# Kernel tuning notes

Hardware: AMD Instinct MI355X
Metric: run time of the kernel (lower is better)

The kernel has to match this reference:

```python
import jax, jax.numpy as jnp
import numpy as np

ZERO = 1e-8
L = 2            # num_gnn_layers
D = 256          # dim_node_features
B = 32           # graphs per batch
NPG = 256        # nodes per graph
N = B * NPG      # total nodes
E = 131072       # edges per edge-type
MAX_TOKENS = 256 # MAX_TOKENS_OF_A_POST
UPD = 0.5        # args.updated_weights_for_A


def _make_edges(k):
    k1, k2, k3 = jax.random.split(k, 3)
    g = jax.random.randint(k1, (E,), 0, B) * NPG          # keep edges within a graph
    src = g + jax.random.randint(k2, (E,), 0, NPG)
    dst = g + jax.random.randint(k3, (E,), 0, NPG)
    return jnp.stack([src, dst]).astype(jnp.int64)


def setup_inputs() -> dict:
    key = jax.random.key(0)
    ks = jax.random.split(key, 12)
    x = jax.random.normal(ks[0], (N, D), dtype=jnp.float32)
    ei_e = _make_edges(ks[1]); ew_e = jax.random.uniform(ks[2], (E,), dtype=jnp.float32)
    ei_p = _make_edges(ks[3]); ew_p = jax.random.uniform(ks[4], (E,), dtype=jnp.float32)
    ei_o = _make_edges(ks[5]); ew_o = jax.random.uniform(ks[6], (E,), dtype=jnp.float32)
    entity_mask = jax.random.randint(ks[7], (B, NPG), 0, 2).astype(bool)
    pattern_mask = jax.random.randint(ks[8], (B, NPG), 0, 2).astype(bool)
    s = 1.0 / np.sqrt(D)
    W_gcn = (jax.random.normal(ks[9], (L, 3, D, D), dtype=jnp.float32) * s)
    b_gcn = jnp.zeros((L, 3, D), dtype=jnp.float32)
    T_dyn = (jax.random.normal(ks[10], (L, D, D), dtype=jnp.float32) * s)
    return {
        'x': x,
        'edge_index_entity': ei_e, 'edge_weight_entity': ew_e,
        'edge_index_pattern': ei_p, 'edge_weight_pattern': ew_p,
        'edge_index_others': ei_o, 'edge_weight_others': ew_o,
        'entity_mask': entity_mask, 'pattern_mask': pattern_mask,
        'W_gcn': W_gcn, 'b_gcn': b_gcn, 'T_dyn': T_dyn,
    }


def _normalized_correlation_matrix(H):
    # cosine-similarity correlation matrix, symmetrically degree-normalized
    nrm = jnp.sqrt(jnp.sum(H * H, axis=1))
    A = (H @ H.T) / (nrm[:, None] * nrm[None, :] + ZERO)
    dinv = 1.0 / jnp.sqrt(jnp.abs(jnp.sum(A, axis=1)) + ZERO)
    return dinv[:, None] * A * dinv[None, :]


def _gcn(H, W, b, ei, ew):
    # GCNConv(add_self_loops=False, normalize=False): scatter-sum of weighted source messages
    msg = (H @ W)[ei[0]] * ew[:, None]                     # [E, D]
    return jax.ops.segment_sum(msg, ei[1], num_segments=N) + b


def _forward(x, we0, wp0, wo0, W_gcn, b_gcn, T_dyn,
             ei_e, ei_p, ei_o, entity_mask, pattern_mask):
    H = x
    A = _normalized_correlation_matrix(H)                  # [N, N]
    for i in range(L):
        if i == 0:
            we, wp, wo = we0, wp0, wo0
        else:
            # diag(one_hot(src) @ A @ one_hot(dst).T) == A[src, dst]
            we = A[ei_e[0], ei_e[1]]
            wp = A[ei_p[0], ei_p[1]]
            wo = A[ei_o[0], ei_o[1]]
        He = _gcn(H, W_gcn[i, 0], b_gcn[i, 0], ei_e, we)
        Hp = _gcn(H, W_gcn[i, 1], b_gcn[i, 1], ei_p, wp)
        Ho = _gcn(H, W_gcn[i, 2], b_gcn[i, 2], ei_o, wo)
        H = jax.nn.relu(He + Hp + Ho)
        A_hat = jax.nn.sigmoid((H @ T_dyn[i]) @ H.T)
        A = (1.0 - UPD) * A + UPD * A_hat
    # per-graph diagonal blocks of A  -> [B, NPG, NPG]
    A4 = A.reshape(B, NPG, B, NPG)
    idx = jnp.arange(B)
    blocks = A4[idx, :, idx, :]
    A_sum = jnp.sum(blocks, axis=-1)                       # [B, NPG]
    ent_cols = jnp.einsum('bij,bj->bi', blocks, entity_mask.astype(A.dtype))
    pat_cols = jnp.einsum('bij,bj->bi', blocks, pattern_mask.astype(A.dtype))
    map_pattern = A_sum - ent_cols
    map_entity = A_sum - pat_cols

    def finish(m):
        mn = jnp.min(m, axis=1, keepdims=True)
        mx = jnp.max(m, axis=1, keepdims=True)
        m = (m - mn) / (mx - mn + ZERO)
        m = m / (jnp.sum(m, axis=1, keepdims=True) + ZERO)
        return m[:, :MAX_TOKENS]                           # padding() with NPG==MAX_TOKENS

    return finish(map_entity), finish(map_pattern)


def reference(x, edge_index_entity, edge_weight_entity,
              edge_index_pattern, edge_weight_pattern,
              edge_index_others, edge_weight_others,
              entity_mask, pattern_mask, W_gcn, b_gcn, T_dyn):
    return _forward(x, edge_weight_entity, edge_weight_pattern, edge_weight_others,
                    W_gcn, b_gcn, T_dyn,
                    edge_index_entity, edge_index_pattern, edge_index_others,
                    entity_mask, pattern_mask)
```

## Files before the change

### kernel.cpp

```cpp
#include <hip/hip_runtime.h>

#define NND   8192
#define DDIM  256
#define NGRP  32
#define ZEROF 1e-8f
#define LSTR  40
#define TSTR  72
#define OFF_AH 0
#define OFF_AL 2560
#define OFF_BH 5120
#define OFF_BL 10240
#define OFF_TT 5120
#define LDS_U16 15360

typedef unsigned short u16;
typedef __attribute__((ext_vector_type(8))) short short8v;
typedef __attribute__((ext_vector_type(4))) float float4v;

__device__ inline u16 f2bf(float x) {
  unsigned u = __float_as_uint(x);
  u += 0x7fffu + ((u >> 16) & 1u);
  return (u16)(u >> 16);
}
__device__ inline float bf2f(u16 h) { return __uint_as_float((unsigned)h << 16); }
__device__ inline void split2(float x, u16& h, u16& l) {
  h = f2bf(x);
  l = f2bf(x - bf2f(h));
}

__device__ inline float wave_sum(float v) {
#pragma unroll
  for (int off = 32; off > 0; off >>= 1) v += __shfl_down(v, off, 64);
  return v;
}

#define LOAD_REGS(tt, kk)                                                                   \
  {                                                                                         \
    int m_ = tid >> 2, kq_ = (tid & 3) * 8;                                                 \
    size_t aoff_;                                                                           \
    if (MODE == 1)                                                                          \
      aoff_ = (size_t)((tt) * 256 + bym * 64 + m_) * 8192 + (size_t)(g * 256 + (kk) + kq_); \
    else if (MODE == 2 || MODE == 3)                                                        \
      aoff_ = (size_t)(g * 256 + bym * 64 + m_) * 256 + (kk) + kq_;                         \
    else                                                                                    \
      aoff_ = (size_t)(bym * 64 + m_) * 256 + (kk) + kq_;                                   \
    rAh = *(const short8v*)&Ah_g[aoff_];                                                    \
    rAl = *(const short8v*)&Al_g[aoff_];                                                    \
    if (MODE == 1) {                                                                        \
      int n_ = tid >> 2, kq2_ = (tid & 3) * 8;                                              \
      const float* pb_ = Bfp + (((size_t)g * 3 + (tt)) << 16) +                             \
                         (size_t)(col0 + n_) * 256 + (kk) + kq2_;                           \
      rBf[0] = *(const float4*)pb_;                                                         \
      rBf[1] = *(const float4*)(pb_ + 4);                                                   \
    } else if (HALF) {                                                                      \
      int n_ = tid & 63, kq2_ = (tid >> 6) * 8;                                             \
      size_t boff_ = (size_t)(((MODE == 2 || MODE == 3) ? g * 256 : 0) + col0 + n_) * 256   \
                     + (kk) + kq2_;                                                         \
      rBh0 = *(const short8v*)&Bh_g[boff_];                                                 \
      rBl0 = *(const short8v*)&Bl_g[boff_];                                                 \
    } else {                                                                                \
      int n_ = tid & 127, kq2_ = (tid >> 7) * 16;                                           \
      size_t boff_ = (size_t)(col0 + n_) * 256 + (kk) + kq2_;                               \
      rBh0 = *(const short8v*)&Bh_g[boff_]; rBh1 = *(const short8v*)&Bh_g[boff_ + 8];       \
      rBl0 = *(const short8v*)&Bl_g[boff_]; rBl1 = *(const short8v*)&Bl_g[boff_ + 8];       \
    }                                                                                       \
  }

template<int MODE, bool HALF>
__device__ __forceinline__ void mfma_body(
    u16* lds,
    const u16* __restrict__ Ah_g, const u16* __restrict__ Al_g,
    const u16* __restrict__ Bh_g, const u16* __restrict__ Bl_g,
    const float* __restrict__ Bfp,
    float* __restrict__ Cf, u16* __restrict__ Ch, u16* __restrict__ Cl,
    const float* __restrict__ nrm, const float* __restrict__ dinv,
    const float* __restrict__ bias,
    int bxm, int bym, int g) {
  u16* Ahs = lds + OFF_AH;
  u16* Als = lds + OFF_AL;
  u16* Bhs = lds + OFF_BH;
  u16* Bls = lds + OFF_BL;
  u16* Tt  = lds + OFF_TT;
  const int NJ = HALF ? 2 : 4;
  const int tid = threadIdx.x;
  const int col0 = bxm * (HALF ? 64 : 128);
  const int w = tid >> 6, lane = tid & 63;
  const int lm = lane & 15, lq = lane >> 4;
  const int wr = (w >> 1) * 32, wc = (w & 1) * (HALF ? 32 : 64);

  float4v acc[2][4];
#pragma unroll
  for (int i = 0; i < 2; ++i)
#pragma unroll
    for (int j = 0; j < NJ; ++j) acc[i][j] = (float4v)0.f;

  short8v rAh, rAl, rBh0, rBh1, rBl0, rBl1;
  float4 rBf[2];
  const int TOTAL = (MODE == 1) ? 24 : 8;

  LOAD_REGS(0, 0);
  for (int step = 0; step < TOTAL; ++step) {
    if (step) __syncthreads();
    {
      int m = tid >> 2, kq = (tid & 3) * 8;
      *(short8v*)&Ahs[m * LSTR + kq] = rAh;
      *(short8v*)&Als[m * LSTR + kq] = rAl;
    }
    if (MODE == 1) {
      int n = tid >> 2, kq2 = (tid & 3) * 8;
      u16 hh[8], ll[8];
      split2(rBf[0].x, hh[0], ll[0]); split2(rBf[0].y, hh[1], ll[1]);
      split2(rBf[0].z, hh[2], ll[2]); split2(rBf[0].w, hh[3], ll[3]);
      split2(rBf[1].x, hh[4], ll[4]); split2(rBf[1].y, hh[5], ll[5]);
      split2(rBf[1].z, hh[6], ll[6]); split2(rBf[1].w, hh[7], ll[7]);
      *(short8v*)&Bhs[n * LSTR + kq2] = *(short8v*)hh;
      *(short8v*)&Bls[n * LSTR + kq2] = *(short8v*)ll;
    } else if (HALF) {
      int n = tid & 63, kq2 = (tid >> 6) * 8;
      *(short8v*)&Bhs[n * LSTR + kq2] = rBh0;
      *(short8v*)&Bls[n * LSTR + kq2] = rBl0;
    } else {
      int n = tid & 127, kq2 = (tid >> 7) * 16;
      *(short8v*)&Bhs[n * LSTR + kq2] = rBh0; *(short8v*)&Bhs[n * LSTR + kq2 + 8] = rBh1;
      *(short8v*)&Bls[n * LSTR + kq2] = rBl0; *(short8v*)&Bls[n * LSTR + kq2 + 8] = rBl1;
    }
    __syncthreads();
    int nxt = step + 1;
    if (nxt < TOTAL) {
      int tt = nxt >> 3, kk = (nxt & 7) * 32;
      LOAD_REGS(tt, kk);
    }
    short8v ah[2], al[2], bh[4], bl[4];
#pragma unroll
    for (int i = 0; i < 2; ++i) {
      int r = wr + i * 16 + lm;
      ah[i] = *(const short8v*)&Ahs[r * LSTR + lq * 8];
      al[i] = *(const short8v*)&Als[r * LSTR + lq * 8];
    }
#pragma unroll
    for (int j = 0; j < NJ; ++j) {
      int r = wc + j * 16 + lm;
      bh[j] = *(const short8v*)&Bhs[r * LSTR + lq * 8];
      bl[j] = *(const short8v*)&Bls[r * LSTR + lq * 8];
    }
#pragma unroll
    for (int i = 0; i < 2; ++i)
#pragma unroll
      for (int j = 0; j < NJ; ++j) {
        acc[i][j] = __builtin_amdgcn_mfma_f32_16x16x32_bf16(ah[i], bh[j], acc[i][j], 0, 0, 0);
        acc[i][j] = __builtin_amdgcn_mfma_f32_16x16x32_bf16(ah[i], bl[j], acc[i][j], 0, 0, 0);
        acc[i][j] = __builtin_amdgcn_mfma_f32_16x16x32_bf16(al[i], bh[j], acc[i][j], 0, 0, 0);
      }
  }

  if (MODE == 2 || MODE == 3) {
#pragma unroll
    for (int i = 0; i < 2; ++i) {
#pragma unroll
      for (int r = 0; r < 4; ++r) {
        int grow = g * 256 + bym * 64 + wr + i * 16 + lq * 4 + r;
        float di = 0.f, ni = 0.f;
        if (MODE == 2) { di = dinv[grow]; ni = nrm[grow]; }
#pragma unroll
        for (int j = 0; j < NJ; ++j) {
          int gcol = col0 + wc + j * 16 + lm;
          size_t ci = (size_t)grow * 256 + gcol;
          float v = acc[i][j][r];
          if (MODE == 2) {
            int gj = g * 256 + gcol;
            Cf[ci] = v * di * dinv[gj] / (ni * nrm[gj] + ZEROF);
          } else {
            Cf[ci] = 0.5f * Cf[ci] + 0.5f * (1.f / (1.f + expf(-v)));
          }
        }
      }
    }
  } else {
    float bsum[8];
    if (MODE == 1) {
#pragma unroll
      for (int i = 0; i < 2; ++i)
#pragma unroll
        for (int r = 0; r < 4; ++r) {
          int d = bym * 64 + wr + i * 16 + lq * 4 + r;
          bsum[i * 4 + r] = bias[d] + bias[256 + d] + bias[512 + d];
        }
    }
    u16 hv[32], lv[32];
#pragma unroll
    for (int i = 0; i < 2; ++i)
#pragma unroll
      for (int j = 0; j < NJ; ++j)
#pragma unroll
        for (int r = 0; r < 4; ++r) {
          float v = acc[i][j][r];
          if (MODE == 1) v = fmaxf(v + bsum[i * 4 + r], 0.f);
          split2(v, hv[(i * 4 + r) * NJ + j], lv[(i * 4 + r) * NJ + j]);
        }
    int ebase1 = (MODE == 1) ? (g * 256 + col0) : col0;
    int ebase2 = bym * 64;
    size_t estride = (MODE == 0) ? 8192 : 256;
#pragma unroll
    for (int ph = 0; ph < 2; ++ph) {
      __syncthreads();
      const u16* sv = ph ? lv : hv;
#pragma unroll
      for (int i = 0; i < 2; ++i)
#pragma unroll
        for (int j = 0; j < NJ; ++j)
#pragma unroll
          for (int r = 0; r < 4; ++r)
            Tt[(wc + j * 16 + lm) * TSTR + wr + i * 16 + lq * 4 + r] = sv[(i * 4 + r) * NJ + j];
      __syncthreads();
      u16* dst = ph ? Cl : Ch;
      int cc0 = tid >> 3, mm0 = (tid & 7) * 8;
#pragma unroll
      for (int it = 0; it < (HALF ? 2 : 4); ++it) {
        int cc = it * 32 + cc0;
        short8v v = *(const short8v*)&Tt[cc * TSTR + mm0];
        *(short8v*)&dst[(size_t)(ebase1 + cc) * estride + ebase2 + mm0] = v;
      }
    }
  }
}

__global__ void k_prep(const int* __restrict__ e0, const int* __restrict__ e1,
                       const int* __restrict__ e2, const unsigned char* __restrict__ m0,
                       const unsigned char* __restrict__ m1,
                       const float* __restrict__ W, const float* __restrict__ T,
                       const float* __restrict__ x,
                       int* __restrict__ eo, float* __restrict__ emf, float* __restrict__ pmf,
                       u16* __restrict__ Wth, u16* __restrict__ Wtl,
                       float* __restrict__ Mzero,
                       float* __restrict__ nrm, float* __restrict__ Spart,
                       u16* __restrict__ Hh, u16* __restrict__ Hl,
                       int E2, int nCvt) {
  __shared__ float tile[32][33];
  __shared__ float inv[64];
  __shared__ int nz[2];
  const int b = blockIdx.x, tid = threadIdx.x;
  if (b < nCvt) {
    if (tid < 2) nz[tid] = 0;
    __syncthreads();
    if (e0[2 * tid + 1] != 0) atomicAdd(&nz[0], 1);
    int i4 = tid * 4;
    int c = (m0[i4 + 1] != 0) + (m0[i4 + 2] != 0) + (m0[i4 + 3] != 0);
    if (c) atomicAdd(&nz[1], c);
    __syncthreads();
    int fE = (nz[0] == 0), fM = (nz[1] == 0);
    int i = b * 256 + tid;
    if (i < E2) {
      eo[i] = fE ? e0[2 * i] : e0[i];
    } else if (i < 2 * E2) {
      int j = i - E2; eo[E2 + j] = fE ? e1[2 * j] : e1[j];
    } else if (i < 3 * E2) {
      int j = i - 2 * E2; eo[2 * E2 + j] = fE ? e2[2 * j] : e2[j];
    } else if (i < 3 * E2 + NND) {
      int j = i - 3 * E2; unsigned char v = fM ? m0[4 * j] : m0[j];
      emf[j] = 1.f - (float)(v != 0);
    } else if (i < 3 * E2 + 2 * NND) {
      int j = i - 3 * E2 - NND; unsigned char v = fM ? m1[4 * j] : m1[j];
      pmf[j] = 1.f - (float)(v != 0);
    }
  } else if (b < nCvt + 512) {
    int bb = b - nCvt;
    int mat = bb >> 6, rem = bb & 63;
    int k0 = (rem >> 3) * 32, n0 = (rem & 7) * 32;
    const float* src = (mat < 6) ? (W + (size_t)mat * 65536) : (T + (size_t)(mat - 6) * 65536);
    int r = tid >> 3, c4 = (tid & 7) * 4;
    const float4 v = *(const float4*)&src[(size_t)(k0 + r) * 256 + n0 + c4];
    tile[r][c4 + 0] = v.x; tile[r][c4 + 1] = v.y; tile[r][c4 + 2] = v.z; tile[r][c4 + 3] = v.w;
    __syncthreads();
    float o[4] = {tile[c4 + 0][r], tile[c4 + 1][r], tile[c4 + 2][r], tile[c4 + 3][r]};
    u16 hh[4], ll[4];
#pragma unroll
    for (int q = 0; q < 4; ++q) split2(o[q], hh[q], ll[q]);
    size_t off = (size_t)mat * 65536 + (size_t)(n0 + r) * 256 + k0 + c4;
    *(ushort4*)&Wth[off] = *(ushort4*)hh;
    *(ushort4*)&Wtl[off] = *(ushort4*)ll;
  } else if (b < nCvt + 512 + 3072) {
    int bb = b - nCvt - 512;
    float4* p = (float4*)Mzero;
    size_t base = (size_t)bb * 1024 + tid;
    float4 z = make_float4(0.f, 0.f, 0.f, 0.f);
    p[base] = z; p[base + 256] = z; p[base + 512] = z; p[base + 768] = z;
  } else {
    int bn = b - nCvt - 512 - 3072;
    int n0 = bn * 64;
    int w = tid >> 6, lane = tid & 63;
    for (int it = 0; it < 16; ++it) {
      int nl = it * 4 + w;
      int node = n0 + nl;
      const float4 v = *(const float4*)&x[(size_t)node * 256 + lane * 4];
      u16 hh[4], ll[4];
      split2(v.x, hh[0], ll[0]); split2(v.y, hh[1], ll[1]);
      split2(v.z, hh[2], ll[2]); split2(v.w, hh[3], ll[3]);
      *(ushort4*)&Hh[(size_t)node * 256 + lane * 4] = *(ushort4*)hh;
      *(ushort4*)&Hl[(size_t)node * 256 + lane * 4] = *(ushort4*)ll;
      float s = wave_sum(v.x * v.x + v.y * v.y + v.z * v.z + v.w * v.w);
      if (lane == 0) { float nr = sqrtf(s); nrm[node] = nr; inv[nl] = 1.f / nr; }
    }
    __syncthreads();
    float s = 0.f;
    for (int i = 0; i < 64; ++i) s += x[(size_t)(n0 + i) * 256 + tid] * inv[i];
    Spart[bn * 256 + tid] = s;
  }
}

__global__ __launch_bounds__(256, 2) void k_stageA(
    const u16* __restrict__ Hinh, const u16* __restrict__ Hinl,
    const u16* __restrict__ Wth, const u16* __restrict__ Wtl, int l,
    u16* __restrict__ XWTh, u16* __restrict__ XWTl,
    const int* __restrict__ edges, const float* __restrict__ ew0,
    const float* __restrict__ ew1, const float* __restrict__ ew2,
    const float* __restrict__ Abuf, float* __restrict__ Mb, int E_,
    const float* __restrict__ x, const float* __restrict__ Spart,
    const float* __restrict__ nrm, float* __restrict__ dinv) {
  __shared__ u16 lds[LDS_U16];
  const int b = blockIdx.x;
  if (b < 768) {
    mfma_body<0, false>(lds, Hinh, Hinl, Wth + (size_t)l * 768 * 256,
                        Wtl + (size_t)l * 768 * 256, nullptr,
                        nullptr, XWTh, XWTl, nullptr, nullptr, nullptr,
                        b >> 7, b & 127, 0);
  } else if (b < 1280) {
    int bi = b - 768;
    for (int i = bi * 256 + threadIdx.x; i < 3 * E_; i += 131072) {
      int t = i / E_;
      int e = i - t * E_;
      const int* ei = edges + (size_t)t * 2 * E_;
      int src = ei[e], dst = ei[E_ + e];
      float wgt = l ? Abuf[(size_t)src * 256 + (dst & 255)]
                    : (t == 0 ? ew0 : (t == 1 ? ew1 : ew2))[e];
      int gg = src >> 8;
      atomicAdd(&Mb[(((size_t)gg * 3 + t) << 16) + ((size_t)(dst & 255) << 8) + (src & 255)],
                wgt);
    }
  } else {
    float* Sl = (float*)lds;
    const int tid = threadIdx.x;
    float s = 0.f;
    for (int bb = 0; bb < 128; ++bb) s += Spart[bb * 256 + tid];
    Sl[tid] = s;
    __syncthreads();
    int base = (b - 1280) * 64;
    int w = tid >> 6, lane = tid & 63;
    const float4 sv = *(const float4*)&Sl[lane * 4];
    for (int it = 0; it < 16; ++it) {
      int node = base + it * 4 + w;
      const float4 v = *(const float4*)&x[(size_t)node * 256 + lane * 4];
      float s2 = wave_sum(v.x * sv.x + v.y * sv.y + v.z * sv.z + v.w * sv.w);
      if (lane == 0) {
        float rowsum = s2 / nrm[node];
        dinv[node] = rsqrtf(fabsf(rowsum) + ZEROF);
      }
    }
  }
}

__global__ __launch_bounds__(256, 2) void k_stageB(
    const u16* __restrict__ XWTh, const u16* __restrict__ XWTl,
    const float* __restrict__ Mb,
    u16* __restrict__ Houth, u16* __restrict__ Houtl, const float* __restrict__ bias,
    const u16* __restrict__ xh, const u16* __restrict__ xl, float* __restrict__ Abuf,
    const float* __restrict__ nrm, const float* __restrict__ dinv) {
  __shared__ u16 lds[LDS_U16];
  const int b = blockIdx.x;
  if (b < 512) {
    int g = b & 31, r = b >> 5;
    mfma_body<1, true>(lds, XWTh, XWTl, nullptr, nullptr, Mb,
                       nullptr, Houth, Houtl, nullptr, nullptr, bias,
                       r >> 2, r & 3, g);
  } else {
    int bb = b - 512;
    int g = bb & 31, r = bb >> 5;
    mfma_body<2, true>(lds, xh, xl, xh, xl, nullptr, Abuf, nullptr, nullptr,
                       nrm, dinv, nullptr, r >> 2, r & 3, g);
  }
}

__global__ __launch_bounds__(256, 2) void k_stageC(
    const u16* __restrict__ Wth, const u16* __restrict__ Wtl, int l,
    const u16* __restrict__ Hh, const u16* __restrict__ Hl,
    u16* __restrict__ tmph, u16* __restrict__ tmpl) {
  __shared__ u16 lds[LDS_U16];
  const int b = blockIdx.x;
  mfma_body<4, true>(lds, Wth + (size_t)(6 + l) * 65536, Wtl + (size_t)(6 + l) * 65536,
                     Hh, Hl, nullptr, nullptr, tmph, tmpl, nullptr, nullptr, nullptr,
                     b & 127, b >> 7, 0);
}

__global__ __launch_bounds__(256, 2) void k_stageD(
    const u16* __restrict__ tmph, const u16* __restrict__ tmpl,
    const u16* __restrict__ Hh, const u16* __restrict__ Hl,
    float* __restrict__ Abuf) {
  __shared__ u16 lds[LDS_U16];
  const int b = blockIdx.x;
  int g = b & 31, r = b >> 5;
  mfma_body<3, true>(lds, tmph, tmpl, Hh, Hl, nullptr, Abuf, nullptr, nullptr,
                     nullptr, nullptr, nullptr, r >> 2, r & 3, g);
}

__global__ void k_maps(const float* __restrict__ Abuf, const float* __restrict__ emf,
                       const float* __restrict__ pmf, float* __restrict__ out) {
  __shared__ float sme[256], smp[256], red[256];
  const int g = blockIdx.x, tid = threadIdx.x, w = tid >> 6, lane = tid & 63;
  const int j0 = g * 256 + lane * 4;
  const float4 pmv = *(const float4*)&pmf[j0];
  const float4 emv = *(const float4*)&emf[j0];
  for (int it = 0; it < 64; ++it) {
    int nl = it * 4 + w;
    const float4 a = *(const float4*)&Abuf[((size_t)g * 256 + nl) * 256 + lane * 4];
    float me = a.x * pmv.x + a.y * pmv.y + a.z * pmv.z + a.w * pmv.w;
    float mp = a.x * emv.x + a.y * emv.y + a.z * emv.z + a.w * emv.w;
#pragma unroll
    for (int off = 32; off > 0; off >>= 1) {
      me += __shfl_down(me, off, 64);
      mp += __shfl_down(mp, off, 64);
    }
    if (lane == 0) { sme[nl] = me; smp[nl] = mp; }
  }
  __syncthreads();
  for (int which = 0; which < 2; ++which) {
    float v = which ? smp[tid] : sme[tid];
    red[tid] = v; __syncthreads();
    for (int s = 128; s > 0; s >>= 1) { if (tid < s) red[tid] = fminf(red[tid], red[tid + s]); __syncthreads(); }
    float mn = red[0]; __syncthreads();
    red[tid] = v; __syncthreads();
    for (int s = 128; s > 0; s >>= 1) { if (tid < s) red[tid] = fmaxf(red[tid], red[tid + s]); __syncthreads(); }
    float mx = red[0]; __syncthreads();
    float m = (v - mn) / (mx - mn + ZEROF);
    red[tid] = m; __syncthreads();
    for (int s = 128; s > 0; s >>= 1) { if (tid < s) red[tid] += red[tid + s]; __syncthreads(); }
    float sum = red[0]; __syncthreads();
    out[which * NND + g * 256 + tid] = m / (sum + ZEROF);
  }
}

extern "C" void kernel_launch(void* const* d_in, const int* in_sizes, int n_in,
                              void* d_out, int out_size, void* d_ws, size_t ws_size,
                              hipStream_t stream) {
  const float* x = (const float*)d_in[0];
  const unsigned char* em_raw = (const unsigned char*)d_in[7];
  const unsigned char* pm_raw = (const unsigned char*)d_in[8];
  const float* W  = (const float*)d_in[9];
  const float* bg = (const float*)d_in[10];
  const float* T  = (const float*)d_in[11];
  float* out = (float*)d_out;
  const int E_ = in_sizes[2];
  const int E2 = 2 * E_;

  float* ws = (float*)d_ws;
  size_t o = 0;
  float* Abuf = ws + o; o += (size_t)NND * 256;
  float* Mb3  = ws + o; o += (size_t)2 * NGRP * 3 * 65536;
  u16* Hh   = (u16*)(ws + o); o += (size_t)NND * 256 / 2;
  u16* Hl   = (u16*)(ws + o); o += (size_t)NND * 256 / 2;
  u16* H2h  = (u16*)(ws + o); o += (size_t)NND * 256 / 2;
  u16* H2l  = (u16*)(ws + o); o += (size_t)NND * 256 / 2;
  u16* tmph = (u16*)(ws + o); o += (size_t)NND * 256 / 2;
  u16* tmpl = (u16*)(ws + o); o += (size_t)NND * 256 / 2;
  u16* XWTh = (u16*)(ws + o); o += (size_t)768 * NND / 2;
  u16* XWTl = (u16*)(ws + o); o += (size_t)768 * NND / 2;
  u16* Wth  = (u16*)(ws + o); o += (size_t)8 * 65536 / 2;
  u16* Wtl  = (u16*)(ws + o); o += (size_t)8 * 65536 / 2;
  float* nrm   = ws + o; o += NND;
  float* dinv  = ws + o; o += NND;
  float* Spart = ws + o; o += 128 * 256;
  float* emf   = ws + o; o += NND;
  float* pmf   = ws + o; o += NND;
  int* edges   = (int*)(ws + o); o += (size_t)3 * E2;

  const float* ew0 = (const float*)d_in[2];
  const float* ew1 = (const float*)d_in[4];
  const float* ew2 = (const float*)d_in[6];
  float* Mb_l0 = Mb3;
  float* Mb_l1 = Mb3 + (size_t)NGRP * 3 * 65536;

  const int nCvt = (3 * E2 + 2 * NND + 255) / 256;

  k_prep<<<nCvt + 512 + 3072 + 128, 256, 0, stream>>>(
      (const int*)d_in[1], (const int*)d_in[3], (const int*)d_in[5], em_raw, pm_raw,
      W, T, x, edges, emf, pmf, Wth, Wtl, Mb3, nrm, Spart, Hh, Hl, E2, nCvt);

  k_stageA<<<1408, 256, 0, stream>>>(Hh, Hl, Wth, Wtl, 0, XWTh, XWTl,
                                     edges, ew0, ew1, ew2, Abuf, Mb_l0, E_,
                                     x, Spart, nrm, dinv);
  k_stageB<<<1024, 256, 0, stream>>>(XWTh, XWTl, Mb_l0, H2h, H2l, bg,
                                     Hh, Hl, Abuf, nrm, dinv);
  k_stageC<<<512, 256, 0, stream>>>(Wth, Wtl, 0, H2h, H2l, tmph, tmpl);
  k_stageD<<<512, 256, 0, stream>>>(tmph, tmpl, H2h, H2l, Abuf);

  k_stageA<<<1280, 256, 0, stream>>>(H2h, H2l, Wth, Wtl, 1, XWTh, XWTl,
                                     edges, ew0, ew1, ew2, Abuf, Mb_l1, E_,
                                     x, Spart, nrm, dinv);
  k_stageB<<<512, 256, 0, stream>>>(XWTh, XWTl, Mb_l1, Hh, Hl, bg + 768,
                                    nullptr, nullptr, nullptr, nullptr, nullptr);
  k_stageC<<<512, 256, 0, stream>>>(Wth, Wtl, 1, Hh, Hl, tmph, tmpl);
  k_stageD<<<512, 256, 0, stream>>>(tmph, tmpl, Hh, Hl, Abuf);

  k_maps<<<NGRP, 256, 0, stream>>>(Abuf, emf, pmf, out);
}
```

Baseline: 281.9 us.

## Bucket edges per graph chunk and accumulate adjacency in LDS tiles

The prep kernel now bins edges by graph, edge type and 32-row destination chunk into fixed-capacity buckets (packed u16 src/dst plus weight). Stage A then builds each 32x256 adjacency slice with shared-memory atomics and writes it out densely. This replaces global-memory atomics and removes the large zero-fill pass over the dense per-graph matrices. The cost is an extra bucketing pass with global counter atomics. It also assumes no bucket exceeds 1024 edges; any excess edges are silently dropped.

```diff
diff --git a/kernel.cpp b/kernel.cpp
--- a/kernel.cpp
+++ b/kernel.cpp
@@ -6,12 +6,13 @@
 #define ZEROF 1e-8f
 #define LSTR  40
 #define TSTR  72
+#define BCAP  1024
 #define OFF_AH 0
 #define OFF_AL 2560
 #define OFF_BH 5120
 #define OFF_BL 10240
 #define OFF_TT 5120
-#define LDS_U16 15360
+#define LDS_U16 16384
 
 typedef unsigned short u16;
 typedef __attribute__((ext_vector_type(8))) short short8v;
@@ -229,41 +230,61 @@
                        const unsigned char* __restrict__ m1,
                        const float* __restrict__ W, const float* __restrict__ T,
                        const float* __restrict__ x,
-                       int* __restrict__ eo, float* __restrict__ emf, float* __restrict__ pmf,
+                       const float* __restrict__ ew0, const float* __restrict__ ew1,
+                       const float* __restrict__ ew2,
+                       float* __restrict__ emf, float* __restrict__ pmf,
                        u16* __restrict__ Wth, u16* __restrict__ Wtl,
-                       float* __restrict__ Mzero,
+                       int* __restrict__ bcnt, u16* __restrict__ bsd,
+                       float* __restrict__ bw0,
                        float* __restrict__ nrm, float* __restrict__ Spart,
                        u16* __restrict__ Hh, u16* __restrict__ Hl,
-                       int E2, int nCvt) {
+                       int E_, int nCvt, int nBkt) {
   __shared__ float tile[32][33];
   __shared__ float inv[64];
-  __shared__ int nz[2];
+  __shared__ int nz[1];
   const int b = blockIdx.x, tid = threadIdx.x;
   if (b < nCvt) {
-    if (tid < 2) nz[tid] = 0;
-    __syncthreads();
-    if (e0[2 * tid + 1] != 0) atomicAdd(&nz[0], 1);
+    if (tid == 0) nz[0] = 0;
+    __syncthreads();
     int i4 = tid * 4;
     int c = (m0[i4 + 1] != 0) + (m0[i4 + 2] != 0) + (m0[i4 + 3] != 0);
-    if (c) atomicAdd(&nz[1], c);
-    __syncthreads();
-    int fE = (nz[0] == 0), fM = (nz[1] == 0);
+    if (c) atomicAdd(&nz[0], c);
+    __syncthreads();
+    int fM = (nz[0] == 0);
     int i = b * 256 + tid;
-    if (i < E2) {
-      eo[i] = fE ? e0[2 * i] : e0[i];
-    } else if (i < 2 * E2) {
-      int j = i - E2; eo[E2 + j] = fE ? e1[2 * j] : e1[j];
-    } else if (i < 3 * E2) {
-      int j = i - 2 * E2; eo[2 * E2 + j] = fE ? e2[2 * j] : e2[j];
-    } else if (i < 3 * E2 + NND) {
-      int j = i - 3 * E2; unsigned char v = fM ? m0[4 * j] : m0[j];
-      emf[j] = 1.f - (float)(v != 0);
-    } else if (i < 3 * E2 + 2 * NND) {
-      int j = i - 3 * E2 - NND; unsigned char v = fM ? m1[4 * j] : m1[j];
+    if (i < NND) {
+      unsigned char v = fM ? m0[4 * i] : m0[i];
+      emf[i] = 1.f - (float)(v != 0);
+    } else {
+      int j = i - NND;
+      unsigned char v = fM ? m1[4 * j] : m1[j];
       pmf[j] = 1.f - (float)(v != 0);
     }
-  } else if (b < nCvt + 512) {
-    int bb = b - nCvt;
+  } else if (b < nCvt + nBkt) {
+    if (tid == 0) nz[0] = 0;
+    __syncthreads();
+    if (e0[2 * tid + 1] != 0) atomicAdd(&nz[0], 1);
+    __syncthreads();
+    int fE = (nz[0] == 0);
+    int e = (b - nCvt) * 256 + tid;
+    if (e < E_) {
+#pragma unroll
+      for (int t = 0; t < 3; ++t) {
+        const int* ei = (t == 0) ? e0 : ((t == 1) ? e1 : e2);
+        int src = fE ? ei[2 * e] : ei[e];
+        int dst = fE ? ei[2 * (E_ + e)] : ei[E_ + e];
+        int g = src >> 8, s = src & 255, d = dst & 255;
+        int bid = ((g * 3 + t) << 3) | (d >> 5);
+        int slot = atomicAdd(&bcnt[bid], 1);
+        if (slot < BCAP) {
+          size_t off = (size_t)bid * BCAP + slot;
+          bsd[off] = (u16)(((d & 31) << 8) | s);
+          bw0[off] = (t == 0 ? ew0 : (t == 1 ? ew1 : ew2))[e];
+        }
+      }
+    }
+  } else if (b < nCvt + nBkt + 512) {
+    int bb = b - nCvt - nBkt;
     int mat = bb >> 6, rem = bb & 63;
     int k0 = (rem >> 3) * 32, n0 = (rem & 7) * 32;
     const float* src = (mat < 6) ? (W + (size_t)mat * 65536) : (T + (size_t)(mat - 6) * 65536);
@@ -278,14 +299,8 @@
     size_t off = (size_t)mat * 65536 + (size_t)(n0 + r) * 256 + k0 + c4;
     *(ushort4*)&Wth[off] = *(ushort4*)hh;
     *(ushort4*)&Wtl[off] = *(ushort4*)ll;
-  } else if (b < nCvt + 512 + 3072) {
-    int bb = b - nCvt - 512;
-    float4* p = (float4*)Mzero;
-    size_t base = (size_t)bb * 1024 + tid;
-    float4 z = make_float4(0.f, 0.f, 0.f, 0.f);
-    p[base] = z; p[base + 256] = z; p[base + 512] = z; p[base + 768] = z;
   } else {
-    int bn = b - nCvt - 512 - 3072;
+    int bn = b - nCvt - nBkt - 512;
     int n0 = bn * 64;
     int w = tid >> 6, lane = tid & 63;
     for (int it = 0; it < 16; ++it) {
@@ -311,9 +326,9 @@
     const u16* __restrict__ Hinh, const u16* __restrict__ Hinl,
     const u16* __restrict__ Wth, const u16* __restrict__ Wtl, int l,
     u16* __restrict__ XWTh, u16* __restrict__ XWTl,
-    const int* __restrict__ edges, const float* __restrict__ ew0,
-    const float* __restrict__ ew1, const float* __restrict__ ew2,
-    const float* __restrict__ Abuf, float* __restrict__ Mb, int E_,
+    const int* __restrict__ bcnt, const u16* __restrict__ bsd,
+    const float* __restrict__ bw0,
+    const float* __restrict__ Abuf, float* __restrict__ Mb,
     const float* __restrict__ x, const float* __restrict__ Spart,
     const float* __restrict__ nrm, float* __restrict__ dinv) {
   __shared__ u16 lds[LDS_U16];
@@ -323,19 +338,29 @@
                         Wtl + (size_t)l * 768 * 256, nullptr,
                         nullptr, XWTh, XWTl, nullptr, nullptr, nullptr,
                         b >> 7, b & 127, 0);
-  } else if (b < 1280) {
-    int bi = b - 768;
-    for (int i = bi * 256 + threadIdx.x; i < 3 * E_; i += 131072) {
-      int t = i / E_;
-      int e = i - t * E_;
-      const int* ei = edges + (size_t)t * 2 * E_;
-      int src = ei[e], dst = ei[E_ + e];
-      float wgt = l ? Abuf[(size_t)src * 256 + (dst & 255)]
-                    : (t == 0 ? ew0 : (t == 1 ? ew1 : ew2))[e];
-      int gg = src >> 8;
-      atomicAdd(&Mb[(((size_t)gg * 3 + t) << 16) + ((size_t)(dst & 255) << 8) + (src & 255)],
-                wgt);
-    }
+  } else if (b < 1536) {
+    const int tid = threadIdx.x;
+    int bid = b - 768;
+    int gt = bid >> 3, chunk = bid & 7;
+    int g = gt / 3;
+    float* tile = (float*)lds;
+    float4 z = make_float4(0.f, 0.f, 0.f, 0.f);
+#pragma unroll
+    for (int k = 0; k < 8; ++k) ((float4*)tile)[k * 256 + tid] = z;
+    __syncthreads();
+    int cnt = bcnt[bid];
+    if (cnt > BCAP) cnt = BCAP;
+    for (int i = tid; i < cnt; i += 256) {
+      size_t off = (size_t)bid * BCAP + i;
+      u16 sd = bsd[off];
+      int s = sd & 255, d5 = sd >> 8;
+      float w = l ? Abuf[(size_t)(g * 256 + s) * 256 + chunk * 32 + d5] : bw0[off];
+      atomicAdd(&tile[d5 * 256 + s], w);
+    }
+    __syncthreads();
+    float4* dst = (float4*)&Mb[((size_t)gt << 16) + ((size_t)chunk << 13)];
+#pragma unroll
+    for (int k = 0; k < 8; ++k) dst[k * 256 + tid] = ((float4*)tile)[k * 256 + tid];
   } else {
     float* Sl = (float*)lds;
     const int tid = threadIdx.x;
@@ -343,7 +368,7 @@
     for (int bb = 0; bb < 128; ++bb) s += Spart[bb * 256 + tid];
     Sl[tid] = s;
     __syncthreads();
-    int base = (b - 1280) * 64;
+    int base = (b - 1536) * 64;
     int w = tid >> 6, lane = tid & 63;
     const float4 sv = *(const float4*)&Sl[lane * 4];
     for (int it = 0; it < 16; ++it) {
@@ -448,7 +473,6 @@
   const float* T  = (const float*)d_in[11];
   float* out = (float*)d_out;
   const int E_ = in_sizes[2];
-  const int E2 = 2 * E_;
 
   float* ws = (float*)d_ws;
   size_t o = 0;
@@ -469,7 +493,9 @@
   float* Spart = ws + o; o += 128 * 256;
   float* emf   = ws + o; o += NND;
   float* pmf   = ws + o; o += NND;
-  int* edges   = (int*)(ws + o); o += (size_t)3 * E2;
+  int* bcnt    = (int*)(ws + o); o += 768;
+  u16* bsd     = (u16*)(ws + o); o += (size_t)768 * BCAP / 2;
+  float* bw0   = ws + o; o += (size_t)768 * BCAP;
 
   const float* ew0 = (const float*)d_in[2];
   const float* ew1 = (const float*)d_in[4];
@@ -477,22 +503,26 @@
   float* Mb_l0 = Mb3;
   float* Mb_l1 = Mb3 + (size_t)NGRP * 3 * 65536;
 
-  const int nCvt = (3 * E2 + 2 * NND + 255) / 256;
-
-  k_prep<<<nCvt + 512 + 3072 + 128, 256, 0, stream>>>(
+  const int nCvt = (2 * NND) / 256;
+  const int nBkt = (E_ + 255) / 256;
+
+  hipMemsetAsync(bcnt, 0, 768 * sizeof(int), stream);
+
+  k_prep<<<nCvt + nBkt + 512 + 128, 256, 0, stream>>>(
       (const int*)d_in[1], (const int*)d_in[3], (const int*)d_in[5], em_raw, pm_raw,
-      W, T, x, edges, emf, pmf, Wth, Wtl, Mb3, nrm, Spart, Hh, Hl, E2, nCvt);
-
-  k_stageA<<<1408, 256, 0, stream>>>(Hh, Hl, Wth, Wtl, 0, XWTh, XWTl,
-                                     edges, ew0, ew1, ew2, Abuf, Mb_l0, E_,
+      W, T, x, ew0, ew1, ew2, emf, pmf, Wth, Wtl, bcnt, bsd, bw0,
+      nrm, Spart, Hh, Hl, E_, nCvt, nBkt);
+
+  k_stageA<<<1664, 256, 0, stream>>>(Hh, Hl, Wth, Wtl, 0, XWTh, XWTl,
+                                     bcnt, bsd, bw0, Abuf, Mb_l0,
                                      x, Spart, nrm, dinv);
   k_stageB<<<1024, 256, 0, stream>>>(XWTh, XWTl, Mb_l0, H2h, H2l, bg,
                                      Hh, Hl, Abuf, nrm, dinv);
   k_stageC<<<512, 256, 0, stream>>>(Wth, Wtl, 0, H2h, H2l, tmph, tmpl);
   k_stageD<<<512, 256, 0, stream>>>(tmph, tmpl, H2h, H2l, Abuf);
 
-  k_stageA<<<1280, 256, 0, stream>>>(H2h, H2l, Wth, Wtl, 1, XWTh, XWTl,
-                                     edges, ew0, ew1, ew2, Abuf, Mb_l1, E_,
+  k_stageA<<<1536, 256, 0, stream>>>(H2h, H2l, Wth, Wtl, 1, XWTh, XWTl,
+                                     bcnt, bsd, bw0, Abuf, Mb_l1,
                                      x, Spart, nrm, dinv);
   k_stageB<<<512, 256, 0, stream>>>(XWTh, XWTl, Mb_l1, Hh, Hl, bg + 768,
                                     nullptr, nullptr, nullptr, nullptr, nullptr);
```

Measured after the change: 356.9 us. 26.6% more time.
